# Performance work log

Hardware: AMD Instinct MI355X
Metric: run time of the kernel (lower is better)

Reference implementation:

```python
import jax, jax.numpy as jnp
import numpy as np

B, S, HID, H = 8, 1024, 2048, 16
D = HID // H  # head dim 128
MAX_LEN, SCALE_BASE, THETA_BASE, EPS = 1024, 512.0, 10000.0, 1e-5


def setup_inputs() -> dict:
    key = jax.random.key(0)
    ks = jax.random.split(key, 10)
    std = 0.02
    n_layers_scale = std / np.sqrt(24.0)
    return {
        "activations": jax.random.normal(ks[0], (B, S, HID), jnp.float32),
        "cache_k": jnp.zeros((B, MAX_LEN, H, D), jnp.float32),
        "cache_v": jnp.zeros((B, MAX_LEN, H, D), jnp.float32),
        "index": 0,
        "ln1_w": jnp.ones((HID,), jnp.float32),
        "ln2_w": jnp.ones((HID,), jnp.float32),
        "q_w": std * jax.random.normal(ks[1], (HID, HID), jnp.float32),
        "k_w": std * jax.random.normal(ks[2], (HID, HID), jnp.float32),
        "v_w": std * jax.random.normal(ks[3], (HID, HID), jnp.float32),
        "o_w": n_layers_scale * jax.random.normal(ks[4], (HID, HID), jnp.float32),
        "w1": std * jax.random.normal(ks[5], (4 * HID, HID), jnp.float32),
        "w2": n_layers_scale * jax.random.normal(ks[6], (HID, 4 * HID), jnp.float32),
    }


def _ln(x, w):
    m = jnp.mean(x, axis=-1, keepdims=True)
    v = jnp.mean((x - m) ** 2, axis=-1, keepdims=True)
    return (x - m) * jax.lax.rsqrt(v + EPS) * w


def _rotate_every_two(x):
    return jnp.stack((-x[..., 1::2], x[..., 0::2]), axis=-1).reshape(x.shape)


def _xpos_consts(start, end):
    drange = jnp.arange(2, D + 2, 2, dtype=jnp.float32)
    theta = jnp.repeat((1.0 / THETA_BASE) ** (drange / D), 2)
    alpha = 0.4 * D
    zeta = jnp.repeat((drange / (D / 2) + alpha) / (1 + alpha), 2)
    half = MAX_LEN // 2
    seq = (jnp.arange(-half, MAX_LEN - half, dtype=jnp.float32) / SCALE_BASE)[start:end]
    seq = seq[:, None, None]  # [S,1,1]
    c = jnp.cos(seq * theta[None, None, :])  # [S,1,D]
    s = jnp.sin(seq * theta[None, None, :])
    t = zeta[None, None, :] ** seq
    return c, s, t


def reference(activations, cache_k, cache_v, index, ln1_w, ln2_w, q_w, k_w, v_w, o_w, w1, w2):
    xn = _ln(activations, ln1_w)
    q = (xn @ q_w.T).reshape(B, S, H, D)
    k = (xn @ k_w.T).reshape(B, S, H, D)
    v = (xn @ v_w.T).reshape(B, S, H, D)
    # NOTE: source applies xpos to (keys, values), exactly as written
    c, s, t = _xpos_consts(index, index + S)
    k = (k * c + _rotate_every_two(k) * s) * t
    v = (v * c + _rotate_every_two(v) * s) / t
    # index==0 and S==MAX_LEN -> get_full_kv returns incoming kv, mask None (causal)
    scale = 1.0 / np.sqrt(D)
    scores = jnp.einsum("bqhd,bkhd->bhqk", q, k) * scale
    causal = jnp.tril(jnp.ones((S, S), bool))
    scores = jnp.where(causal[None, None], scores, -jnp.inf)
    attn = jax.nn.softmax(scores, axis=-1)
    ctx = jnp.einsum("bhqk,bkhd->bqhd", attn, v).reshape(B, S, HID)
    acts = activations + ctx @ o_w.T
    h = jax.nn.gelu(_ln(acts, ln2_w) @ w1.T, approximate=False)
    acts = acts + h @ w2.T
    return acts, cache_k, cache_v
```

## Files before the change

### kernel.cpp

```cpp
#include <hip/hip_runtime.h>
#include <hip/hip_bf16.h>
#include <math.h>

#define B_ 8
#define S_ 1024
#define HID_ 2048
#define H_ 16
#define D_ 128

typedef __attribute__((ext_vector_type(8))) short bf16x8;
typedef __attribute__((ext_vector_type(4))) float f32x4;

__device__ inline unsigned short f2b_raw(float f){
  union { __hip_bfloat16 h; unsigned short u; } cv; cv.h = __float2bfloat16(f); return cv.u;
}

__device__ inline void async_copy16(const void* g, void* l){
  __builtin_amdgcn_global_load_lds((const __attribute__((address_space(1))) unsigned int*)g,
                                   (__attribute__((address_space(3))) unsigned int*)l, 16, 0, 0);
}

__global__ __launch_bounds__(256) void cvt_all(const float* __restrict__ qw, const float* __restrict__ kw,
                                               const float* __restrict__ vw, const float* __restrict__ ow,
                                               const float* __restrict__ w1, const float* __restrict__ w2,
                                               unsigned short* __restrict__ dst){
  int i = blockIdx.x*256 + threadIdx.x;
  if (i >= 12582912) return;
  const float* src;
  int local;
  if      (i <  1048576){ src = qw; local = i; }
  else if (i <  2097152){ src = kw; local = i - 1048576; }
  else if (i <  3145728){ src = vw; local = i - 2097152; }
  else if (i <  4194304){ src = ow; local = i - 3145728; }
  else if (i <  8388608){ src = w1; local = i - 4194304; }
  else                  { src = w2; local = i - 8388608; }
  float4 f = ((const float4*)src)[local];
  ushort4 o;
  o.x = f2b_raw(f.x); o.y = f2b_raw(f.y); o.z = f2b_raw(f.z); o.w = f2b_raw(f.w);
  ((ushort4*)dst)[i] = o;
}

__global__ __launch_bounds__(256) void ln_kernel(const float* __restrict__ x,
                                                 const float* __restrict__ w,
                                                 unsigned short* __restrict__ y){
  const int row = blockIdx.x, tid = threadIdx.x;
  const float* xr = x + (size_t)row*HID_;
  float4 a = ((const float4*)xr)[tid];
  float4 b = ((const float4*)xr)[tid+256];
  float s  = a.x+a.y+a.z+a.w + b.x+b.y+b.z+b.w;
  float ss = a.x*a.x+a.y*a.y+a.z*a.z+a.w*a.w + b.x*b.x+b.y*b.y+b.z*b.z+b.w*b.w;
  #pragma unroll
  for (int off=1; off<64; off<<=1){ s += __shfl_xor(s, off, 64); ss += __shfl_xor(ss, off, 64); }
  __shared__ float red[8];
  int wv = tid>>6;
  if ((tid&63)==0){ red[wv]=s; red[4+wv]=ss; }
  __syncthreads();
  s  = red[0]+red[1]+red[2]+red[3];
  ss = red[4]+red[5]+red[6]+red[7];
  float mean = s * (1.0f/HID_);
  float var  = ss * (1.0f/HID_) - mean*mean;
  float rstd = rsqrtf(var + 1e-5f);
  float4 w0 = ((const float4*)w)[tid];
  float4 w1v = ((const float4*)w)[tid+256];
  ushort4 o0, o1;
  o0.x = f2b_raw((a.x-mean)*rstd*w0.x); o0.y = f2b_raw((a.y-mean)*rstd*w0.y);
  o0.z = f2b_raw((a.z-mean)*rstd*w0.z); o0.w = f2b_raw((a.w-mean)*rstd*w0.w);
  o1.x = f2b_raw((b.x-mean)*rstd*w1v.x); o1.y = f2b_raw((b.y-mean)*rstd*w1v.y);
  o1.z = f2b_raw((b.z-mean)*rstd*w1v.z); o1.w = f2b_raw((b.w-mean)*rstd*w1v.w);
  *(ushort4*)(y + (size_t)row*HID_ + tid*4) = o0;
  *(ushort4*)(y + (size_t)row*HID_ + 1024 + tid*4) = o1;
}

#define STAGE_A(ch, kk, dst) { async_copy16(Ab + sOffA[ch][0] + (kk), (dst) + sLdsA[ch][0]); \
                               async_copy16(Ab + sOffA[ch][1] + (kk), (dst) + sLdsA[ch][1]); }
#define STAGE_B(ch, kk, dst) { async_copy16(Wb + sOffB[ch][0] + (kk), (dst) + sLdsB[ch][0]); \
                               async_copy16(Wb + sOffB[ch][1] + (kk), (dst) + sLdsB[ch][1]); }

template<int EPI, int TAG>
__global__ __launch_bounds__(512, 2) void gemm_bt(
    const unsigned short* __restrict__ A, const unsigned short* __restrict__ W,
    unsigned short* __restrict__ out_b, float* __restrict__ out_f,
    const float* __restrict__ res,
    unsigned short* __restrict__ k_out, unsigned short* __restrict__ vt_out,
    const int* __restrict__ idxp,
    int M, int N, int K, float scale)
{
  (void)M;
  __shared__ __align__(16) unsigned short smem[65536];
  const int tid = threadIdx.x;
  const int lane = tid & 63, wv = tid >> 6;
  const int wm = wv >> 2, wn = wv & 3;
  const int lm = lane & 15, lg = lane >> 4;

  const int gx = gridDim.x;
  const int nwg = gx * gridDim.y;
  const int orig = blockIdx.y * gx + blockIdx.x;
  const int wg = (orig & 7) * (nwg >> 3) + (orig >> 3);
  const int bx = wg % gx, by = wg / gx;
  const int m0 = by << 8, n0 = bx << 8;

  f32x4 acc[8][4];
  #pragma unroll
  for (int r=0;r<8;r++)
    #pragma unroll
    for (int c=0;c<4;c++) acc[r][c] = (f32x4){0.f,0.f,0.f,0.f};

  int oA[2], oB[2];
  #pragma unroll
  for (int kc=0;kc<2;kc++){
    const int swz = ((kc*4+lg) ^ (lm&7)) * 8;
    oA[kc] = wm*8192 + lm*64 + swz;
    oB[kc] = wn*4096 + lm*64 + swz;
  }

  int sOffA[2][2], sLdsA[2][2], sOffB[2][2], sLdsB[2][2];
  #pragma unroll
  for (int j=0;j<2;j++){
    const int unit = j*512 + tid;
    const int r7 = unit >> 3, u = unit & 7;
    const int r7g = (unit & ~63) >> 3;
    #pragma unroll
    for (int ch=0; ch<2; ch++){
      const int rowA  = (r7  & 63) + ((r7  & 64) << 1) + ch*64;
      const int rowA0 = (r7g & 63) + ((r7g & 64) << 1) + ch*64;
      sOffA[ch][j] = rowA*K + (u ^ (rowA & 7))*8;
      sLdsA[ch][j] = __builtin_amdgcn_readfirstlane(rowA0*64);
      const int rowB  = (r7  & 31) + ((r7  & 96) << 1) + ch*32;
      const int rowB0 = (r7g & 31) + ((r7g & 96) << 1) + ch*32;
      sOffB[ch][j] = rowB*K + (u ^ (rowB & 7))*8;
      sLdsB[ch][j] = __builtin_amdgcn_readfirstlane(rowB0*64);
    }
  }

  const unsigned short* Ab = A + (size_t)m0 * K;
  const unsigned short* Wb = W + (size_t)n0 * K;
  const unsigned short* sA0 = smem;
  const unsigned short* sB0 = smem + 16384;
  const unsigned short* sA1 = smem + 32768;
  const unsigned short* sB1 = smem + 49152;
  unsigned short* dA0 = smem;
  unsigned short* dB0 = smem + 16384;
  unsigned short* dA1 = smem + 32768;
  unsigned short* dB1 = smem + 49152;

  STAGE_A(0, 0, dA0);
  STAGE_B(0, 0, dB0);
  STAGE_B(1, 0, dB0);
  STAGE_A(1, 0, dA0);
  STAGE_A(0, 64, dA1);
  STAGE_B(0, 64, dB1);
  STAGE_B(1, 64, dB1);

  const int T2 = K >> 7;
  bf16x8 a[4][2], b[4][2];

  for (int it=0; it<T2; ++it){
    const int o1 = (2*it+1) << 6;
    const int e2 = (2*it+2) << 6;
    const int o2 = (2*it+3) << 6;
    const bool pf = (it+1 < T2);

    asm volatile("s_waitcnt vmcnt(6)\n\ts_barrier" ::: "memory");
    #pragma unroll
    for (int r=0;r<4;r++)
      #pragma unroll
      for (int kc=0;kc<2;kc++)
        a[r][kc] = *(const bf16x8*)(sA0 + oA[kc] + r*1024);
    #pragma unroll
    for (int c=0;c<2;c++)
      #pragma unroll
      for (int kc=0;kc<2;kc++)
        b[c][kc] = *(const bf16x8*)(sB0 + oB[kc] + c*1024);
    STAGE_A(1, o1, dA1);
    __builtin_amdgcn_sched_barrier(0);
    __builtin_amdgcn_s_setprio(1);
    #pragma unroll
    for (int r=0;r<4;r++)
      #pragma unroll
      for (int c=0;c<2;c++)
        #pragma unroll
        for (int kc=0;kc<2;kc++)
          acc[r][c] = __builtin_amdgcn_mfma_f32_16x16x32_bf16(a[r][kc], b[c][kc], acc[r][c], 0,0,0);
    __builtin_amdgcn_s_setprio(0);

    asm volatile("s_barrier" ::: "memory");
    #pragma unroll
    for (int c=0;c<2;c++)
      #pragma unroll
      for (int kc=0;kc<2;kc++)
        b[2+c][kc] = *(const bf16x8*)(sB0 + oB[kc] + (2+c)*1024);
    if (pf) STAGE_A(0, e2, dA0);
    __builtin_amdgcn_sched_barrier(0);
    __builtin_amdgcn_s_setprio(1);
    #pragma unroll
    for (int r=0;r<4;r++)
      #pragma unroll
      for (int c=0;c<2;c++)
        #pragma unroll
        for (int kc=0;kc<2;kc++)
          acc[r][2+c] = __builtin_amdgcn_mfma_f32_16x16x32_bf16(a[r][kc], b[2+c][kc], acc[r][2+c], 0,0,0);
    __builtin_amdgcn_s_setprio(0);

    asm volatile("s_barrier" ::: "memory");
    #pragma unroll
    for (int r=0;r<4;r++)
      #pragma unroll
      for (int kc=0;kc<2;kc++)
        a[r][kc] = *(const bf16x8*)(sA0 + oA[kc] + 4096 + r*1024);
    if (pf) STAGE_B(0, e2, dB0);
    __builtin_amdgcn_sched_barrier(0);
    __builtin_amdgcn_s_setprio(1);
    #pragma unroll
    for (int r=0;r<4;r++)
      #pragma unroll
      for (int c=0;c<2;c++)
        #pragma unroll
        for (int kc=0;kc<2;kc++)
          acc[4+r][2+c] = __builtin_amdgcn_mfma_f32_16x16x32_bf16(a[r][kc], b[2+c][kc], acc[4+r][2+c], 0,0,0);
    __builtin_amdgcn_s_setprio(0);

    asm volatile("s_barrier" ::: "memory");
    if (pf) STAGE_B(1, e2, dB0);
    __builtin_amdgcn_sched_barrier(0);
    __builtin_amdgcn_s_setprio(1);
    #pragma unroll
    for (int r=0;r<4;r++)
      #pragma unroll
      for (int c=0;c<2;c++)
        #pragma unroll
        for (int kc=0;kc<2;kc++)
          acc[4+r][c] = __builtin_amdgcn_mfma_f32_16x16x32_bf16(a[r][kc], b[c][kc], acc[4+r][c], 0,0,0);
    __builtin_amdgcn_s_setprio(0);

    if (pf){ asm volatile("s_waitcnt vmcnt(6)\n\ts_barrier" ::: "memory"); }
    else   { asm volatile("s_waitcnt vmcnt(0)\n\ts_barrier" ::: "memory"); }
    #pragma unroll
    for (int r=0;r<4;r++)
      #pragma unroll
      for (int kc=0;kc<2;kc++)
        a[r][kc] = *(const bf16x8*)(sA1 + oA[kc] + r*1024);
    #pragma unroll
    for (int c=0;c<2;c++)
      #pragma unroll
      for (int kc=0;kc<2;kc++)
        b[c][kc] = *(const bf16x8*)(sB1 + oB[kc] + c*1024);
    if (pf) STAGE_A(1, e2, dA0);
    __builtin_amdgcn_sched_barrier(0);
    __builtin_amdgcn_s_setprio(1);
    #pragma unroll
    for (int r=0;r<4;r++)
      #pragma unroll
      for (int c=0;c<2;c++)
        #pragma unroll
        for (int kc=0;kc<2;kc++)
          acc[r][c] = __builtin_amdgcn_mfma_f32_16x16x32_bf16(a[r][kc], b[c][kc], acc[r][c], 0,0,0);
    __builtin_amdgcn_s_setprio(0);

    asm volatile("s_barrier" ::: "memory");
    #pragma unroll
    for (int c=0;c<2;c++)
      #pragma unroll
      for (int kc=0;kc<2;kc++)
        b[2+c][kc] = *(const bf16x8*)(sB1 + oB[kc] + (2+c)*1024);
    if (pf) STAGE_A(0, o2, dA1);
    __builtin_amdgcn_sched_barrier(0);
    __builtin_amdgcn_s_setprio(1);
    #pragma unroll
    for (int r=0;r<4;r++)
      #pragma unroll
      for (int c=0;c<2;c++)
        #pragma unroll
        for (int kc=0;kc<2;kc++)
          acc[r][2+c] = __builtin_amdgcn_mfma_f32_16x16x32_bf16(a[r][kc], b[2+c][kc], acc[r][2+c], 0,0,0);
    __builtin_amdgcn_s_setprio(0);

    asm volatile("s_barrier" ::: "memory");
    #pragma unroll
    for (int r=0;r<4;r++)
      #pragma unroll
      for (int kc=0;kc<2;kc++)
        a[r][kc] = *(const bf16x8*)(sA1 + oA[kc] + 4096 + r*1024);
    if (pf) STAGE_B(0, o2, dB1);
    __builtin_amdgcn_sched_barrier(0);
    __builtin_amdgcn_s_setprio(1);
    #pragma unroll
    for (int r=0;r<4;r++)
      #pragma unroll
      for (int c=0;c<2;c++)
        #pragma unroll
        for (int kc=0;kc<2;kc++)
          acc[4+r][2+c] = __builtin_amdgcn_mfma_f32_16x16x32_bf16(a[r][kc], b[2+c][kc], acc[4+r][2+c], 0,0,0);
    __builtin_amdgcn_s_setprio(0);

    asm volatile("s_barrier" ::: "memory");
    if (pf) STAGE_B(1, o2, dB1);
    __builtin_amdgcn_sched_barrier(0);
    __builtin_amdgcn_s_setprio(1);
    #pragma unroll
    for (int r=0;r<4;r++)
      #pragma unroll
      for (int c=0;c<2;c++)
        #pragma unroll
        for (int kc=0;kc<2;kc++)
          acc[4+r][c] = __builtin_amdgcn_mfma_f32_16x16x32_bf16(a[r][kc], b[c][kc], acc[4+r][c], 0,0,0);
    __builtin_amdgcn_s_setprio(0);
  }

  if (EPI == 0){
    const int region = n0 >> 11;
    const int idx0 = idxp[0];
    const int b  = m0 >> 10;
    const int s0g = m0 & 1023;
    const int hh = ((n0 & 2047) >> 7) + (wn >> 1);
    const int db = (wn & 1) * 64;
    #pragma unroll
    for (int r=0;r<8;r++){
      #pragma unroll
      for (int c=0;c<4;c++){
        const int srow = s0g + wm*128 + r*16 + lg*4;
        const int d = db + c*16 + lm;
        if (region == 0){
          #pragma unroll
          for (int g=0; g<4; g++)
            out_b[(((size_t)b*H_ + hh)*S_ + srow + g)*D_ + d] = f2b_raw(acc[r][c][g]*scale);
        } else {
          const float fp = (float)((d>>1) + 1);
          const float theta = exp2f(fp * -0.2076205059304601f);
          const float zeta  = (fp*0.03125f + 51.2f) * (1.0f/52.2f);
          const float lz = log2f(zeta);
          const float sgn = (d & 1) ? 1.0f : -1.0f;
          #pragma unroll
          for (int g=0; g<4; g++){
            float va = acc[r][c][g];
            float part = __shfl_xor(va, 1, 64);
            float seq = ((float)(idx0 + srow + g) - 512.0f) * (1.0f/512.0f);
            float ang = seq * theta;
            float sn, cc;
            __sincosf(ang, &sn, &cc);
            float rot = va*cc + sgn*part*sn;
            if (region == 1){
              float tt = exp2f(seq * lz);
              k_out[(((size_t)b*H_ + hh)*S_ + srow + g)*D_ + d] = f2b_raw(rot * tt);
            } else {
              float ti = exp2f(-seq * lz);
              int d_local = wn*64 + c*16 + lm;
              int s_local = wm*128 + r*16 + lg*4 + g;
              int s8 = s_local >> 3;
              smem[d_local*256 + ((s8 ^ (d_local & 7))*8) + (s_local & 7)] = f2b_raw(rot * ti);
            }
          }
        }
      }
    }
    if (region == 2){
      __syncthreads();
      #pragma unroll
      for (int i=0;i<16;i++){
        int f = i*512 + tid;
        int dl = f >> 5, u = f & 31;
        int us = u ^ (dl & 7);
        uint4 val = *(const uint4*)(smem + dl*256 + us*8);
        int hh2 = ((n0 & 2047) >> 7) + (dl >> 7);
        *(uint4*)(vt_out + ((size_t)((size_t)b*H_ + hh2)*D_ + (dl & 127))*S_ + s0g + u*8) = val;
      }
    }
  } else {
    #pragma unroll
    for (int r=0;r<8;r++){
      #pragma unroll
      for (int c=0;c<4;c++){
        const int row0 = m0 + wm*128 + r*16 + lg*4;
        const int col  = n0 + wn*64 + c*16 + lm;
        #pragma unroll
        for (int g=0; g<4; g++){
          float vacc = acc[r][c][g];
          size_t o = (size_t)(row0 + g)*N + col;
          if (EPI == 1){
            out_f[o] = vacc + res[o];
          } else {
            out_b[o] = f2b_raw(0.5f*vacc*(1.0f + erff(vacc*0.70710678118654752f)));
          }
        }
      }
    }
  }
}

__global__ __launch_bounds__(256) void flash_attn(
    const unsigned short* __restrict__ Q, const unsigned short* __restrict__ Kx,
    const unsigned short* __restrict__ VT, unsigned short* __restrict__ ctx)
{
  __shared__ unsigned short sK[64*136];
  __shared__ unsigned short sVT[128*72];
  __shared__ unsigned short sP[4][16*72];
  const int tid = threadIdx.x, lane = tid & 63, wv = tid >> 6;
  const int lm = lane & 15, lg = lane >> 4;
  const int qt = blockIdx.x, bh = blockIdx.y;
  const size_t base = (size_t)bh * S_ * D_;
  const int qr = qt*64 + wv*16;

  bf16x8 aq[4];
  #pragma unroll
  for (int kc=0;kc<4;kc++)
    aq[kc] = *(const bf16x8*)(Q + base + (size_t)(qr + lm)*D_ + kc*32 + lg*8);

  f32x4 accO[8];
  #pragma unroll
  for (int n=0;n<8;n++) accO[n] = (f32x4){0.f,0.f,0.f,0.f};
  float mrow[4] = {-INFINITY,-INFINITY,-INFINITY,-INFINITY};
  float lrow[4] = {0.f,0.f,0.f,0.f};
  unsigned short* myP = &sP[wv][0];

  for (int kt=0; kt<=qt; ++kt){
    int k0 = kt*64;
    __syncthreads();
    #pragma unroll
    for (int i=0;i<4;i++){
      int chunk = i*256 + tid;
      int krow = chunk >> 4, c8 = chunk & 15;
      *(uint4*)(sK + krow*136 + c8*8) = *(const uint4*)(Kx + base + (size_t)(k0+krow)*D_ + c8*8);
      int dd = chunk >> 3, c4 = chunk & 7;
      *(uint4*)(sVT + dd*72 + c4*8) = *(const uint4*)(VT + base + (size_t)dd*S_ + k0 + c4*8);
    }
    __syncthreads();
    f32x4 sc[4];
    #pragma unroll
    for (int n=0;n<4;n++){
      sc[n] = (f32x4){0.f,0.f,0.f,0.f};
      #pragma unroll
      for (int kc=0;kc<4;kc++){
        bf16x8 bk = *(const bf16x8*)(sK + (n*16+lm)*136 + kc*32 + lg*8);
        sc[n] = __builtin_amdgcn_mfma_f32_16x16x32_bf16(aq[kc], bk, sc[n], 0,0,0);
      }
    }
    if (kt == qt){
      #pragma unroll
      for (int n=0;n<4;n++)
        #pragma unroll
        for (int g=0; g<4; g++)
          if (k0 + n*16 + lm > qr + lg*4 + g) sc[n][g] = -INFINITY;
    }
    float mnew[4], alpha[4];
    #pragma unroll
    for (int g=0; g<4; g++){
      float mx = fmaxf(fmaxf(sc[0][g], sc[1][g]), fmaxf(sc[2][g], sc[3][g]));
      #pragma unroll
      for (int off=1; off<16; off<<=1) mx = fmaxf(mx, __shfl_xor(mx, off, 16));
      mnew[g] = fmaxf(mrow[g], mx);
      alpha[g] = __expf(mrow[g] - mnew[g]);
      mrow[g] = mnew[g];
    }
    #pragma unroll
    for (int n=0;n<4;n++)
      #pragma unroll
      for (int g=0; g<4; g++)
        sc[n][g] = __expf(sc[n][g] - mnew[g]);
    #pragma unroll
    for (int g=0; g<4; g++){
      float sum = sc[0][g]+sc[1][g]+sc[2][g]+sc[3][g];
      #pragma unroll
      for (int off=1; off<16; off<<=1) sum += __shfl_xor(sum, off, 16);
      lrow[g] = lrow[g]*alpha[g] + sum;
    }
    #pragma unroll
    for (int n=0;n<8;n++)
      #pragma unroll
      for (int g=0; g<4; g++) accO[n][g] *= alpha[g];
    #pragma unroll
    for (int n=0;n<4;n++)
      #pragma unroll
      for (int g=0; g<4; g++)
        myP[(lg*4+g)*72 + n*16 + lm] = f2b_raw(sc[n][g]);
    #pragma unroll
    for (int kc=0;kc<2;kc++){
      bf16x8 ap = *(const bf16x8*)(myP + lm*72 + kc*32 + lg*8);
      #pragma unroll
      for (int n=0;n<8;n++){
        bf16x8 bv = *(const bf16x8*)(sVT + (n*16+lm)*72 + kc*32 + lg*8);
        accO[n] = __builtin_amdgcn_mfma_f32_16x16x32_bf16(ap, bv, accO[n], 0,0,0);
      }
    }
  }
  const int b = bh >> 4, hh = bh & 15;
  float rl[4];
  #pragma unroll
  for (int g=0; g<4; g++) rl[g] = 1.0f / lrow[g];
  #pragma unroll
  for (int n=0;n<8;n++)
    #pragma unroll
    for (int g=0; g<4; g++){
      int srow = qr + lg*4 + g;
      int d = n*16 + lm;
      ctx[(((size_t)b*S_ + srow)*H_ + hh)*D_ + d] = f2b_raw(accO[n][g]*rl[g]);
    }
}

extern "C" void kernel_launch(void* const* d_in, const int* in_sizes, int n_in,
                              void* d_out, int out_size, void* d_ws, size_t ws_size,
                              hipStream_t stream)
{
  (void)in_sizes; (void)n_in; (void)out_size; (void)ws_size;
  const float* acts   = (const float*)d_in[0];
  const float* cachek = (const float*)d_in[1];
  const float* cachev = (const float*)d_in[2];
  const int*   idxp   = (const int*)d_in[3];
  const float* ln1w   = (const float*)d_in[4];
  const float* ln2w   = (const float*)d_in[5];
  const float* qw     = (const float*)d_in[6];
  const float* kw     = (const float*)d_in[7];
  const float* vw     = (const float*)d_in[8];
  const float* ow     = (const float*)d_in[9];
  const float* w1     = (const float*)d_in[10];
  const float* w2     = (const float*)d_in[11];
  float* out = (float*)d_out;

  unsigned short* wqkv = (unsigned short*)d_ws;
  unsigned short* wo_b = wqkv + 12582912;
  unsigned short* w1_b = wo_b + 4194304;
  unsigned short* w2_b = w1_b + 16777216;
  unsigned short* xn   = w2_b + 16777216;
  unsigned short* qws  = xn   + 16777216;
  unsigned short* kws  = qws  + 16777216;
  unsigned short* vtws = kws  + 16777216;
  unsigned short* ctx  = vtws + 16777216;
  unsigned short* hbuf = qws;

  cvt_all<<<49152, 256, 0, stream>>>(qw, kw, vw, ow, w1, w2, wqkv);

  ln_kernel<<<8192, 256, 0, stream>>>(acts, ln1w, xn);

  gemm_bt<0,0><<<dim3(24,32), 512, 0, stream>>>(xn, wqkv, qws, nullptr, nullptr,
                                                kws, vtws, idxp,
                                                8192, 6144, 2048, 0.08838834764831845f);

  flash_attn<<<dim3(16,128), 256, 0, stream>>>(qws, kws, vtws, ctx);

  gemm_bt<1,1><<<dim3(8,32), 512, 0, stream>>>(ctx, wo_b, nullptr, out, acts,
                                               nullptr, nullptr, nullptr,
                                               8192, 2048, 2048, 1.0f);

  ln_kernel<<<8192, 256, 0, stream>>>(out, ln2w, xn);

  gemm_bt<2,2><<<dim3(32,32), 512, 0, stream>>>(xn, w1_b, hbuf, nullptr, nullptr,
                                                nullptr, nullptr, nullptr,
                                                8192, 8192, 2048, 1.0f);

  gemm_bt<1,3><<<dim3(8,32), 512, 0, stream>>>(hbuf, w2_b, nullptr, out, out,
                                               nullptr, nullptr, nullptr,
                                               8192, 2048, 8192, 1.0f);

  hipMemcpyAsync(out + 16777216, cachek, 67108864ull, hipMemcpyDeviceToDevice, stream);
  hipMemcpyAsync(out + 33554432, cachev, 67108864ull, hipMemcpyDeviceToDevice, stream);
}
```

Before: 1.578 ms.

## Restructure GEMM main-loop barriers and LDS waits around MFMA quads

Reorders the 8-wave GEMM ping-pong loop so each MFMA quad is followed by a barrier, and adds explicit lgkmcnt waits plus a barrier before each quad so LDS reads complete under a shared sync point. The initial vmcnt wait moves out of the loop into the prologue, and the last B stage is issued just before the vmcnt barrier instead of a separate phase. The MFMA order is also changed to iterate kc outermost. The goal is tighter overlap of LDS reads, async global-to-LDS copies and MFMA issue across waves. The extra barriers could add stalls, and the altered waitcnt placement risks races if counts are wrong.

```diff
diff --git a/kernel.cpp b/kernel.cpp
--- a/kernel.cpp
+++ b/kernel.cpp
@@ -150,9 +150,24 @@
   STAGE_A(0, 64, dA1);
   STAGE_B(0, 64, dB1);
   STAGE_B(1, 64, dB1);
+  asm volatile("s_waitcnt vmcnt(6)\n\ts_barrier" ::: "memory");
 
   const int T2 = K >> 7;
   bf16x8 a[4][2], b[4][2];
+
+  #define MFMA_QUAD(AIDX, BOFF)                                                            \
+    __builtin_amdgcn_sched_barrier(0);                                                     \
+    __builtin_amdgcn_s_setprio(1);                                                         \
+    _Pragma("unroll")                                                                      \
+    for (int kc=0;kc<2;kc++)                                                               \
+      _Pragma("unroll")                                                                    \
+      for (int r=0;r<4;r++)                                                                \
+        _Pragma("unroll")                                                                  \
+        for (int c=0;c<2;c++)                                                              \
+          acc[AIDX+r][BOFF+c] = __builtin_amdgcn_mfma_f32_16x16x32_bf16(                   \
+              a[r][kc], b[BOFF+c][kc], acc[AIDX+r][BOFF+c], 0,0,0);                        \
+    __builtin_amdgcn_s_setprio(0);                                                         \
+    asm volatile("s_barrier" ::: "memory");
 
   for (int it=0; it<T2; ++it){
     const int o1 = (2*it+1) << 6;
@@ -160,7 +175,6 @@
     const int o2 = (2*it+3) << 6;
     const bool pf = (it+1 < T2);
 
-    asm volatile("s_waitcnt vmcnt(6)\n\ts_barrier" ::: "memory");
     #pragma unroll
     for (int r=0;r<4;r++)
       #pragma unroll
@@ -172,68 +186,32 @@
       for (int kc=0;kc<2;kc++)
         b[c][kc] = *(const bf16x8*)(sB0 + oB[kc] + c*1024);
     STAGE_A(1, o1, dA1);
-    __builtin_amdgcn_sched_barrier(0);
-    __builtin_amdgcn_s_setprio(1);
-    #pragma unroll
-    for (int r=0;r<4;r++)
-      #pragma unroll
-      for (int c=0;c<2;c++)
-        #pragma unroll
-        for (int kc=0;kc<2;kc++)
-          acc[r][c] = __builtin_amdgcn_mfma_f32_16x16x32_bf16(a[r][kc], b[c][kc], acc[r][c], 0,0,0);
-    __builtin_amdgcn_s_setprio(0);
-
-    asm volatile("s_barrier" ::: "memory");
+    asm volatile("s_waitcnt lgkmcnt(8)\n\ts_barrier\n\ts_waitcnt lgkmcnt(0)" ::: "memory");
+    MFMA_QUAD(0, 0)
+
     #pragma unroll
     for (int c=0;c<2;c++)
       #pragma unroll
       for (int kc=0;kc<2;kc++)
         b[2+c][kc] = *(const bf16x8*)(sB0 + oB[kc] + (2+c)*1024);
     if (pf) STAGE_A(0, e2, dA0);
-    __builtin_amdgcn_sched_barrier(0);
-    __builtin_amdgcn_s_setprio(1);
-    #pragma unroll
-    for (int r=0;r<4;r++)
-      #pragma unroll
-      for (int c=0;c<2;c++)
-        #pragma unroll
-        for (int kc=0;kc<2;kc++)
-          acc[r][2+c] = __builtin_amdgcn_mfma_f32_16x16x32_bf16(a[r][kc], b[2+c][kc], acc[r][2+c], 0,0,0);
-    __builtin_amdgcn_s_setprio(0);
-
-    asm volatile("s_barrier" ::: "memory");
+    asm volatile("s_barrier\n\ts_waitcnt lgkmcnt(0)" ::: "memory");
+    MFMA_QUAD(0, 2)
+
     #pragma unroll
     for (int r=0;r<4;r++)
       #pragma unroll
       for (int kc=0;kc<2;kc++)
         a[r][kc] = *(const bf16x8*)(sA0 + oA[kc] + 4096 + r*1024);
     if (pf) STAGE_B(0, e2, dB0);
-    __builtin_amdgcn_sched_barrier(0);
-    __builtin_amdgcn_s_setprio(1);
-    #pragma unroll
-    for (int r=0;r<4;r++)
-      #pragma unroll
-      for (int c=0;c<2;c++)
-        #pragma unroll
-        for (int kc=0;kc<2;kc++)
-          acc[4+r][2+c] = __builtin_amdgcn_mfma_f32_16x16x32_bf16(a[r][kc], b[2+c][kc], acc[4+r][2+c], 0,0,0);
-    __builtin_amdgcn_s_setprio(0);
-
-    asm volatile("s_barrier" ::: "memory");
-    if (pf) STAGE_B(1, e2, dB0);
-    __builtin_amdgcn_sched_barrier(0);
-    __builtin_amdgcn_s_setprio(1);
-    #pragma unroll
-    for (int r=0;r<4;r++)
-      #pragma unroll
-      for (int c=0;c<2;c++)
-        #pragma unroll
-        for (int kc=0;kc<2;kc++)
-          acc[4+r][c] = __builtin_amdgcn_mfma_f32_16x16x32_bf16(a[r][kc], b[c][kc], acc[4+r][c], 0,0,0);
-    __builtin_amdgcn_s_setprio(0);
-
-    if (pf){ asm volatile("s_waitcnt vmcnt(6)\n\ts_barrier" ::: "memory"); }
+    asm volatile("s_barrier\n\ts_waitcnt lgkmcnt(0)" ::: "memory");
+    MFMA_QUAD(4, 2)
+
+    if (pf){ STAGE_B(1, e2, dB0);
+             asm volatile("s_waitcnt vmcnt(6)\n\ts_barrier" ::: "memory"); }
     else   { asm volatile("s_waitcnt vmcnt(0)\n\ts_barrier" ::: "memory"); }
+    MFMA_QUAD(4, 0)
+
     #pragma unroll
     for (int r=0;r<4;r++)
       #pragma unroll
@@ -245,66 +223,33 @@
       for (int kc=0;kc<2;kc++)
         b[c][kc] = *(const bf16x8*)(sB1 + oB[kc] + c*1024);
     if (pf) STAGE_A(1, e2, dA0);
-    __builtin_amdgcn_sched_barrier(0);
-    __builtin_amdgcn_s_setprio(1);
-    #pragma unroll
-    for (int r=0;r<4;r++)
-      #pragma unroll
-      for (int c=0;c<2;c++)
-        #pragma unroll
-        for (int kc=0;kc<2;kc++)
-          acc[r][c] = __builtin_amdgcn_mfma_f32_16x16x32_bf16(a[r][kc], b[c][kc], acc[r][c], 0,0,0);
-    __builtin_amdgcn_s_setprio(0);
-
-    asm volatile("s_barrier" ::: "memory");
+    asm volatile("s_waitcnt lgkmcnt(8)\n\ts_barrier\n\ts_waitcnt lgkmcnt(0)" ::: "memory");
+    MFMA_QUAD(0, 0)
+
     #pragma unroll
     for (int c=0;c<2;c++)
       #pragma unroll
       for (int kc=0;kc<2;kc++)
         b[2+c][kc] = *(const bf16x8*)(sB1 + oB[kc] + (2+c)*1024);
     if (pf) STAGE_A(0, o2, dA1);
-    __builtin_amdgcn_sched_barrier(0);
-    __builtin_amdgcn_s_setprio(1);
-    #pragma unroll
-    for (int r=0;r<4;r++)
-      #pragma unroll
-      for (int c=0;c<2;c++)
-        #pragma unroll
-        for (int kc=0;kc<2;kc++)
-          acc[r][2+c] = __builtin_amdgcn_mfma_f32_16x16x32_bf16(a[r][kc], b[2+c][kc], acc[r][2+c], 0,0,0);
-    __builtin_amdgcn_s_setprio(0);
-
-    asm volatile("s_barrier" ::: "memory");
+    asm volatile("s_barrier\n\ts_waitcnt lgkmcnt(0)" ::: "memory");
+    MFMA_QUAD(0, 2)
+
     #pragma unroll
     for (int r=0;r<4;r++)
       #pragma unroll
       for (int kc=0;kc<2;kc++)
         a[r][kc] = *(const bf16x8*)(sA1 + oA[kc] + 4096 + r*1024);
     if (pf) STAGE_B(0, o2, dB1);
-    __builtin_amdgcn_sched_barrier(0);
-    __builtin_amdgcn_s_setprio(1);
-    #pragma unroll
-    for (int r=0;r<4;r++)
-      #pragma unroll
-      for (int c=0;c<2;c++)
-        #pragma unroll
-        for (int kc=0;kc<2;kc++)
-          acc[4+r][2+c] = __builtin_amdgcn_mfma_f32_16x16x32_bf16(a[r][kc], b[2+c][kc], acc[4+r][2+c], 0,0,0);
-    __builtin_amdgcn_s_setprio(0);
-
-    asm volatile("s_barrier" ::: "memory");
-    if (pf) STAGE_B(1, o2, dB1);
-    __builtin_amdgcn_sched_barrier(0);
-    __builtin_amdgcn_s_setprio(1);
-    #pragma unroll
-    for (int r=0;r<4;r++)
-      #pragma unroll
-      for (int c=0;c<2;c++)
-        #pragma unroll
-        for (int kc=0;kc<2;kc++)
-          acc[4+r][c] = __builtin_amdgcn_mfma_f32_16x16x32_bf16(a[r][kc], b[c][kc], acc[4+r][c], 0,0,0);
-    __builtin_amdgcn_s_setprio(0);
+    asm volatile("s_barrier\n\ts_waitcnt lgkmcnt(0)" ::: "memory");
+    MFMA_QUAD(4, 2)
+
+    if (pf){ STAGE_B(1, o2, dB1);
+             asm volatile("s_waitcnt vmcnt(6)\n\ts_barrier" ::: "memory"); }
+    else   { asm volatile("s_barrier" ::: "memory"); }
+    MFMA_QUAD(4, 0)
   }
+  #undef MFMA_QUAD
 
   if (EPI == 0){
     const int region = n0 >> 11;
```

Result: no change. 1.579 ms (+0.0%).
